# Kernel optimization log

Measured on AMD Instinct MI355X. Metric: run time of the kernel, lower is better.

Reference implementation:

```python
import jax, jax.numpy as jnp
import numpy as np

B = 128            # trees per batch
D = 6              # complete binary tree depth
NPT = 2 ** (D + 1) - 1   # 127 nodes per tree
H = 450            # JTNN hidden size
V = 780            # junction-tree vocab size


def _build_forest():
    # complete binary trees; node 0 of each tree is the root
    child = np.arange(1, NPT)
    parent = (child - 1) // 2
    offs = (np.arange(B) * NPT)[:, None]
    ch = (child[None, :] + offs).ravel()
    pa = (parent[None, :] + offs).ravel()
    Eup = B * (NPT - 1)
    E = 2 * Eup
    # up (child->parent) edges first, then down (parent->child); +1 dummy pad row
    src = np.concatenate([ch, pa, [0]]).astype(np.int32)
    dst = np.concatenate([pa, ch, [0]]).astype(np.int32)
    rev = np.concatenate([np.arange(Eup) + Eup, np.arange(Eup), [E]]).astype(np.int32)
    depth_child = np.floor(np.log2(child + 1)).astype(np.int64)  # 1..D
    toff = np.arange(B)[:, None] * (NPT - 1)
    rows = []
    for d in range(D, 0, -1):        # bottom-up: deepest child level first
        t = np.nonzero(depth_child == d)[0]
        rows.append((t[None, :] + toff).ravel())
    for d in range(1, D + 1):        # top-down
        t = np.nonzero(depth_child == d)[0]
        rows.append((t[None, :] + toff).ravel() + Eup)
    Lmax = max(len(r) for r in rows)
    sched = np.full((len(rows), Lmax), E, dtype=np.int32)   # pad with dummy id E
    for i, r in enumerate(rows):
        sched[i, :len(r)] = r
    return src, dst, rev, sched


def setup_inputs() -> dict:
    key = jax.random.key(0)
    ks = jax.random.split(key, 8)
    src, dst, rev, sched = _build_forest()
    n_nodes = B * NPT
    p = lambda k, shp: jax.random.normal(k, shp, jnp.float32) * 0.05
    return {
        'wid': jax.random.randint(ks[0], (n_nodes,), 0, V).astype(jnp.int32),
        'src': jnp.asarray(src), 'dst': jnp.asarray(dst), 'rev': jnp.asarray(rev),
        'sched': jnp.asarray(sched),
        'emb': p(ks[1], (V, H)),
        'Wz': p(ks[2], (2 * H, H)), 'bz': jnp.zeros((H,), jnp.float32),
        'Wr': p(ks[3], (H, H)),
        'Ur': p(ks[4], (H, H)), 'bur': jnp.zeros((H,), jnp.float32),
        'Wh': p(ks[5], (2 * H, H)), 'bh': jnp.zeros((H,), jnp.float32),
        'Wg': p(ks[6], (2 * H, H)), 'bg': jnp.zeros((H,), jnp.float32),
    }


def _forward(wid, src, dst, rev, sched, emb, Wz, bz, Wr, Ur, bur, Wh, bh, Wg, bg):
    n_nodes = wid.shape[0]
    E = src.shape[0] - 1              # last slot is a dummy pad row
    x = emb[wid]                      # [N, H] node embeddings
    m = jnp.zeros((E + 1, x.shape[1]), x.dtype)   # edge messages (line-graph node state)
    rm = jnp.zeros_like(m)
    dstE = dst[:E]
    for lvl in range(sched.shape[0]):             # static number of tree levels
        eid = sched[lvl]                          # [Lmax], padded with E
        # pull: s/accum_rm = sum over predecessor line-graph nodes, i.e.
        # sum of m over in-edges of src[e] minus the backtracking (reverse) edge
        node_m = jax.ops.segment_sum(m[:E], dstE, num_segments=n_nodes)
        node_rm = jax.ops.segment_sum(rm[:E], dstE, num_segments=n_nodes)
        se, de = src[eid], dst[eid]
        s = node_m[se] - m[rev[eid]]
        arm = node_rm[se] - rm[rev[eid]]
        sx, dx = x[se], x[de]
        # GRUUpdate (DGL JTNN)
        z = jax.nn.sigmoid(jnp.concatenate([sx, s], 1) @ Wz + bz)
        mt = jnp.tanh(jnp.concatenate([sx, arm], 1) @ Wh + bh)
        m_new = (1.0 - z) * s + z * mt
        r = jax.nn.sigmoid(dx @ Wr + m_new @ Ur + bur)   # W_r has no bias
        m = m.at[eid].set(m_new)
        rm = rm.at[eid].set(r * m_new)
    # update_all: gather messages into destination nodes, then EncoderGatherUpdate
    node_m = jax.ops.segment_sum(m[:E], dstE, num_segments=n_nodes)
    h = jax.nn.relu(jnp.concatenate([x, node_m], 1) @ Wg + bg)   # [N, H]
    return h


def reference(wid, src, dst, rev, sched, emb, Wz, bz, Wr, Ur, bur, Wh, bh, Wg, bg):
    # returns h for all nodes; root_vecs = h[node_offsets] (roots are every NPT-th node)
    return _forward(wid, src, dst, rev, sched, emb, Wz, bz, Wr, Ur, bur, Wh, bh, Wg, bg)
```

## Files before the change

kernel.cpp:

```cpp
#include <hip/hip_runtime.h>
#include <math.h>

#define NTREES 128
#define NPT 127
#define NNODES (NTREES*NPT)
#define EUP (NTREES*(NPT-1))
#define HDIM 450
#define HP 512
#define LMAX 8192
#define NLVL 12

typedef unsigned short u16;
typedef __attribute__((ext_vector_type(8))) short bf16x8;
typedef __attribute__((ext_vector_type(4))) float f32x4;

__device__ __forceinline__ float sigmoidf_(float x) { return 1.f / (1.f + expf(-x)); }
__device__ __forceinline__ u16 f2b(float x) {
  unsigned u = __float_as_uint(x);
  return (u16)((u + 0x7FFFu + ((u >> 16) & 1u)) >> 16);
}
__device__ __forceinline__ float b2f(u16 h) { return __uint_as_float(((unsigned)h) << 16); }
__device__ __forceinline__ bf16x8 sub8(bf16x8 a, bf16x8 b) {
  bf16x8 r;
#pragma unroll
  for (int i = 0; i < 8; ++i) r[i] = (short)f2b(b2f((u16)a[i]) - b2f((u16)b[i]));
  return r;
}

__device__ __forceinline__ u16* ldsp(u16* base, int row, int slot) {
  return base + row * 64 + ((slot ^ (row & 7)) << 3);
}
#define MFMA(a, b, c) __builtin_amdgcn_mfma_f32_16x16x32_bf16(a, b, c, 0, 0, 0)

__device__ __forceinline__ void swz_tiles(int bid, int Mt, int& nt, int& mt) {
  if (Mt & 7) { nt = bid & 7; mt = bid >> 3; }
  else { int xcd = bid & 7; int q = bid >> 3; nt = q & 7; mt = (q & ~7) | xcd; }
}

__global__ void zero_ws(float4* __restrict__ p, int n4) {
  int i = blockIdx.x * 256 + threadIdx.x;
  int stride = gridDim.x * 256;
  for (; i < n4; i += stride) p[i] = make_float4(0.f, 0.f, 0.f, 0.f);
}

__global__ void prep_pad(const float* __restrict__ Wz, const float* __restrict__ Wh,
                         const float* __restrict__ Wr, const float* __restrict__ Ur,
                         const float* __restrict__ Wg,
                         const float* __restrict__ bz, const float* __restrict__ bh,
                         const float* __restrict__ bur, const float* __restrict__ bg,
                         u16* __restrict__ WpreT, u16* __restrict__ WzbT,
                         u16* __restrict__ WhbT, u16* __restrict__ UrT,
                         u16* __restrict__ WgT, float* __restrict__ biasp) {
  int idx = blockIdx.x * 256 + threadIdx.x;
  if (idx < 1536 * 512) {
    int n = idx >> 9, k = idx & 511;
    int sel = n >> 9, j = n & 511;
    float v = 0.f;
    if (k < HDIM && j < HDIM) {
      const float* W = (sel == 0) ? Wz : (sel == 1) ? Wh : Wr;
      v = W[k * HDIM + j];
    }
    WpreT[idx] = f2b(v);
    return;
  }
  idx -= 1536 * 512;
  if (idx < 3 * 262144) {
    int which = idx >> 18; int r = idx & 262143;
    int n = r >> 9, k = r & 511;
    float v = 0.f;
    if (k < HDIM && n < HDIM)
      v = (which == 0) ? Wz[(HDIM + k) * HDIM + n]
        : (which == 1) ? Wh[(HDIM + k) * HDIM + n]
                       : Ur[k * HDIM + n];
    ((which == 0) ? WzbT : (which == 1) ? WhbT : UrT)[r] = f2b(v);
    return;
  }
  idx -= 3 * 262144;
  if (idx < 512 * 1024) {
    int n = idx >> 10, k = idx & 1023;
    float v = 0.f;
    if (n < HDIM) {
      if (k < HDIM) v = Wg[k * HDIM + n];
      else if (k >= HP && (k - HP) < HDIM) v = Wg[(HDIM + k - HP) * HDIM + n];
    }
    WgT[idx] = f2b(v);
    return;
  }
  idx -= 512 * 1024;
  if (idx < 4 * HP) {
    int which = idx >> 9, j = idx & 511;
    float v = 0.f;
    if (j < HDIM)
      v = ((which == 0) ? bz : (which == 1) ? bh : (which == 2) ? bur : bg)[j];
    biasp[idx] = v;
  }
}

__global__ void gather_embed(const int* __restrict__ wid, const float* __restrict__ emb,
                             u16* __restrict__ xp) {
  int gid = blockIdx.x * 256 + threadIdx.x;
  if (gid >= NNODES * 64) return;
  int row = gid >> 6, g = gid & 63;
  int j0 = g * 8;
  const float* er = emb + (size_t)wid[row] * HDIM;
  float f[8] = {0.f, 0.f, 0.f, 0.f, 0.f, 0.f, 0.f, 0.f};
  if (j0 <= 440) {
#pragma unroll
    for (int q = 0; q < 4; ++q) {
      float2 p = *(const float2*)(er + j0 + q * 2);
      f[q * 2] = p.x; f[q * 2 + 1] = p.y;
    }
  } else if (j0 == 448) {
    f[0] = er[448]; f[1] = er[449];
  }
  bf16x8 v;
#pragma unroll
  for (int q = 0; q < 8; ++q) v[q] = (short)f2b(f[q]);
  *(bf16x8*)(xp + (size_t)row * HP + j0) = v;
}

__global__ __launch_bounds__(256, 4) void mfma_pre(
    const u16* __restrict__ xp, const u16* __restrict__ WpreT,
    u16* __restrict__ Xzh, u16* __restrict__ Xr) {
  __shared__ u16 Al[64 * 64], Bl[64 * 64];
  int bid = blockIdx.x;
  int xcd = bid & 7, q0 = bid >> 3;
  int nt = q0 % 24;
  int mt = (q0 / 24) * 8 + xcd;
  if (mt >= NNODES / 64) return;
  int n0 = nt * 64, m0 = mt * 64;
  int tid = threadIdx.x;
  int l = tid & 63, w = tid >> 6, wr = w >> 1, wc = w & 1, lr = l & 15, lq = l >> 4;
  int sr = tid >> 2, skc = tid & 3;
  const u16* abase = xp + (size_t)(m0 + sr) * HP + skc * 16;
  const u16* bbase = WpreT + (size_t)(n0 + sr) * HP + skc * 16;
  f32x4 acc[2][2] = {};
  for (int kt = 0; kt < HP; kt += 64) {
    *(bf16x8*)ldsp(Al, sr, 2 * skc) = ((const bf16x8*)(abase + kt))[0];
    *(bf16x8*)ldsp(Al, sr, 2 * skc + 1) = ((const bf16x8*)(abase + kt))[1];
    *(bf16x8*)ldsp(Bl, sr, 2 * skc) = ((const bf16x8*)(bbase + kt))[0];
    *(bf16x8*)ldsp(Bl, sr, 2 * skc + 1) = ((const bf16x8*)(bbase + kt))[1];
    __syncthreads();
#pragma unroll
    for (int kk = 0; kk < 64; kk += 32) {
      int slot = (kk >> 3) + lq;
      bf16x8 fa0 = *(bf16x8*)ldsp(Al, wr * 32 + lr, slot);
      bf16x8 fa1 = *(bf16x8*)ldsp(Al, wr * 32 + 16 + lr, slot);
      bf16x8 fb0 = *(bf16x8*)ldsp(Bl, wc * 32 + lr, slot);
      bf16x8 fb1 = *(bf16x8*)ldsp(Bl, wc * 32 + 16 + lr, slot);
      acc[0][0] = MFMA(fa0, fb0, acc[0][0]); acc[0][1] = MFMA(fa0, fb1, acc[0][1]);
      acc[1][0] = MFMA(fa1, fb0, acc[1][0]); acc[1][1] = MFMA(fa1, fb1, acc[1][1]);
    }
    __syncthreads();
  }
#pragma unroll
  for (int fi = 0; fi < 2; ++fi)
#pragma unroll
    for (int fj = 0; fj < 2; ++fj) {
      int colg = n0 + wc * 32 + fj * 16 + lr;
#pragma unroll
      for (int reg = 0; reg < 4; ++reg) {
        int row = m0 + wr * 32 + fi * 16 + lq * 4 + reg;
        u16 o = f2b(acc[fi][fj][reg]);
        if (colg < 1024) Xzh[(size_t)row * 1024 + colg] = o;
        else Xr[(size_t)row * HP + (colg - 1024)] = o;
      }
    }
}

__global__ void leaf_lvl0(const int* __restrict__ sched0, const int* __restrict__ src,
                          const u16* __restrict__ Xzh, const float* __restrict__ biasp,
                          u16* __restrict__ mup) {
  int gid = blockIdx.x * 256 + threadIdx.x;
  int r = gid >> 7, g = gid & 127;
  int e = sched0[r];
  int se = src[e];
  int col = g * 4;
  ushort4 xz = *(const ushort4*)(Xzh + (size_t)se * 1024 + col);
  ushort4 xh = *(const ushort4*)(Xzh + (size_t)se * 1024 + 512 + col);
  float4 bz = *(const float4*)(biasp + col);
  float4 bh = *(const float4*)(biasp + 512 + col);
  ushort4 o;
  o.x = f2b(sigmoidf_(b2f(xz.x) + bz.x) * tanhf(b2f(xh.x) + bh.x));
  o.y = f2b(sigmoidf_(b2f(xz.y) + bz.y) * tanhf(b2f(xh.y) + bh.y));
  o.z = f2b(sigmoidf_(b2f(xz.z) + bz.z) * tanhf(b2f(xh.z) + bh.z));
  o.w = f2b(sigmoidf_(b2f(xz.w) + bz.w) * tanhf(b2f(xh.w) + bh.w));
  *(ushort4*)(mup + (size_t)e * HP + col) = o;
}

__global__ __launch_bounds__(256, 4) void mfma_lvl1_up(
    const int* __restrict__ schedrow, const int* __restrict__ src,
    const u16* __restrict__ node_m, const u16* __restrict__ node_rm,
    const u16* __restrict__ Xzh, const u16* __restrict__ WzbT,
    const u16* __restrict__ WhbT, const float* __restrict__ biasp,
    u16* __restrict__ mup) {
  __shared__ u16 Asl[64 * 64], Aal[64 * 64], Bzl[64 * 64], Btl[64 * 64];
  __shared__ int e_s[64], se_s[64];
  int nt, mt;
  swz_tiles(blockIdx.x, gridDim.x >> 3, nt, mt);
  int n0 = nt * 64, m0 = mt * 64;
  int tid = threadIdx.x;
  if (tid < 64) { int e = schedrow[m0 + tid]; e_s[tid] = e; se_s[tid] = src[e]; }
  __syncthreads();
  int l = tid & 63, w = tid >> 6, wr = w >> 1, wc = w & 1, lr = l & 15, lq = l >> 4;
  int sr = tid >> 2, skc = tid & 3;
  int se_st = se_s[sr];
  const u16* pmb = node_m + (size_t)se_st * HP + skc * 16;
  const u16* prb = node_rm + (size_t)se_st * HP + skc * 16;
  const u16* bzb = WzbT + (size_t)(n0 + sr) * HP + skc * 16;
  const u16* btb = WhbT + (size_t)(n0 + sr) * HP + skc * 16;
  f32x4 accZ[2][2] = {}, accT[2][2] = {};
  for (int kt = 0; kt < HP; kt += 64) {
    *(bf16x8*)ldsp(Asl, sr, 2 * skc) = ((const bf16x8*)(pmb + kt))[0];
    *(bf16x8*)ldsp(Asl, sr, 2 * skc + 1) = ((const bf16x8*)(pmb + kt))[1];
    *(bf16x8*)ldsp(Aal, sr, 2 * skc) = ((const bf16x8*)(prb + kt))[0];
    *(bf16x8*)ldsp(Aal, sr, 2 * skc + 1) = ((const bf16x8*)(prb + kt))[1];
    *(bf16x8*)ldsp(Bzl, sr, 2 * skc) = ((const bf16x8*)(bzb + kt))[0];
    *(bf16x8*)ldsp(Bzl, sr, 2 * skc + 1) = ((const bf16x8*)(bzb + kt))[1];
    *(bf16x8*)ldsp(Btl, sr, 2 * skc) = ((const bf16x8*)(btb + kt))[0];
    *(bf16x8*)ldsp(Btl, sr, 2 * skc + 1) = ((const bf16x8*)(btb + kt))[1];
    __syncthreads();
#pragma unroll
    for (int kk = 0; kk < 64; kk += 32) {
      int slot = (kk >> 3) + lq;
      bf16x8 a0 = *(bf16x8*)ldsp(Asl, wr * 32 + lr, slot);
      bf16x8 a1 = *(bf16x8*)ldsp(Asl, wr * 32 + 16 + lr, slot);
      bf16x8 c0 = *(bf16x8*)ldsp(Aal, wr * 32 + lr, slot);
      bf16x8 c1 = *(bf16x8*)ldsp(Aal, wr * 32 + 16 + lr, slot);
      bf16x8 z0 = *(bf16x8*)ldsp(Bzl, wc * 32 + lr, slot);
      bf16x8 z1 = *(bf16x8*)ldsp(Bzl, wc * 32 + 16 + lr, slot);
      bf16x8 t0 = *(bf16x8*)ldsp(Btl, wc * 32 + lr, slot);
      bf16x8 t1 = *(bf16x8*)ldsp(Btl, wc * 32 + 16 + lr, slot);
      accZ[0][0] = MFMA(a0, z0, accZ[0][0]); accZ[0][1] = MFMA(a0, z1, accZ[0][1]);
      accZ[1][0] = MFMA(a1, z0, accZ[1][0]); accZ[1][1] = MFMA(a1, z1, accZ[1][1]);
      accT[0][0] = MFMA(c0, t0, accT[0][0]); accT[0][1] = MFMA(c0, t1, accT[0][1]);
      accT[1][0] = MFMA(c1, t0, accT[1][0]); accT[1][1] = MFMA(c1, t1, accT[1][1]);
    }
    __syncthreads();
  }
#pragma unroll
  for (int fi = 0; fi < 2; ++fi)
#pragma unroll
    for (int fj = 0; fj < 2; ++fj) {
      int colg = n0 + wc * 32 + fj * 16 + lr;
#pragma unroll
      for (int reg = 0; reg < 4; ++reg) {
        int row = wr * 32 + fi * 16 + lq * 4 + reg;
        int e = e_s[row], se = se_s[row];
        float xz = b2f(Xzh[(size_t)se * 1024 + colg]);
        float xh = b2f(Xzh[(size_t)se * 1024 + 512 + colg]);
        float sv = b2f(node_m[(size_t)se * HP + colg]);
        float z = sigmoidf_(accZ[fi][fj][reg] + xz + biasp[colg]);
        float t = tanhf(accT[fi][fj][reg] + xh + biasp[512 + colg]);
        mup[(size_t)e * HP + colg] = f2b((1.f - z) * sv + z * t);
      }
    }
}

__global__ __launch_bounds__(256, 4) void mfma_lvl1_down(
    const int* __restrict__ schedrow, const int* __restrict__ src,
    const u16* __restrict__ node_m, const u16* __restrict__ node_rm,
    const u16* __restrict__ mup, const u16* __restrict__ rmup,
    const u16* __restrict__ Xzh, const u16* __restrict__ WzbT,
    const u16* __restrict__ WhbT, const float* __restrict__ biasp,
    u16* __restrict__ dtmp) {
  __shared__ u16 Asl[64 * 64], Aal[64 * 64], Bzl[64 * 64], Btl[64 * 64];
  __shared__ int se_s[64], eu_s[64];
  int nt, mt;
  swz_tiles(blockIdx.x, gridDim.x >> 3, nt, mt);
  int n0 = nt * 64, m0 = mt * 64;
  int tid = threadIdx.x;
  if (tid < 64) { int e = schedrow[m0 + tid]; eu_s[tid] = e - EUP; se_s[tid] = src[e]; }
  __syncthreads();
  int l = tid & 63, w = tid >> 6, wr = w >> 1, wc = w & 1, lr = l & 15, lq = l >> 4;
  int sr = tid >> 2, skc = tid & 3;
  int se_st = se_s[sr], eu_st = eu_s[sr];
  const u16* pmb = node_m + (size_t)se_st * HP + skc * 16;
  const u16* pub = mup + (size_t)eu_st * HP + skc * 16;
  const u16* prb = node_rm + (size_t)se_st * HP + skc * 16;
  const u16* pvb = rmup + (size_t)eu_st * HP + skc * 16;
  const u16* bzb = WzbT + (size_t)(n0 + sr) * HP + skc * 16;
  const u16* btb = WhbT + (size_t)(n0 + sr) * HP + skc * 16;
  f32x4 accZ[2][2] = {}, accT[2][2] = {};
  for (int kt = 0; kt < HP; kt += 64) {
    *(bf16x8*)ldsp(Asl, sr, 2 * skc) = sub8(((const bf16x8*)(pmb + kt))[0], ((const bf16x8*)(pub + kt))[0]);
    *(bf16x8*)ldsp(Asl, sr, 2 * skc + 1) = sub8(((const bf16x8*)(pmb + kt))[1], ((const bf16x8*)(pub + kt))[1]);
    *(bf16x8*)ldsp(Aal, sr, 2 * skc) = sub8(((const bf16x8*)(prb + kt))[0], ((const bf16x8*)(pvb + kt))[0]);
    *(bf16x8*)ldsp(Aal, sr, 2 * skc + 1) = sub8(((const bf16x8*)(prb + kt))[1], ((const bf16x8*)(pvb + kt))[1]);
    *(bf16x8*)ldsp(Bzl, sr, 2 * skc) = ((const bf16x8*)(bzb + kt))[0];
    *(bf16x8*)ldsp(Bzl, sr, 2 * skc + 1) = ((const bf16x8*)(bzb + kt))[1];
    *(bf16x8*)ldsp(Btl, sr, 2 * skc) = ((const bf16x8*)(btb + kt))[0];
    *(bf16x8*)ldsp(Btl, sr, 2 * skc + 1) = ((const bf16x8*)(btb + kt))[1];
    __syncthreads();
#pragma unroll
    for (int kk = 0; kk < 64; kk += 32) {
      int slot = (kk >> 3) + lq;
      bf16x8 a0 = *(bf16x8*)ldsp(Asl, wr * 32 + lr, slot);
      bf16x8 a1 = *(bf16x8*)ldsp(Asl, wr * 32 + 16 + lr, slot);
      bf16x8 c0 = *(bf16x8*)ldsp(Aal, wr * 32 + lr, slot);
      bf16x8 c1 = *(bf16x8*)ldsp(Aal, wr * 32 + 16 + lr, slot);
      bf16x8 z0 = *(bf16x8*)ldsp(Bzl, wc * 32 + lr, slot);
      bf16x8 z1 = *(bf16x8*)ldsp(Bzl, wc * 32 + 16 + lr, slot);
      bf16x8 t0 = *(bf16x8*)ldsp(Btl, wc * 32 + lr, slot);
      bf16x8 t1 = *(bf16x8*)ldsp(Btl, wc * 32 + 16 + lr, slot);
      accZ[0][0] = MFMA(a0, z0, accZ[0][0]); accZ[0][1] = MFMA(a0, z1, accZ[0][1]);
      accZ[1][0] = MFMA(a1, z0, accZ[1][0]); accZ[1][1] = MFMA(a1, z1, accZ[1][1]);
      accT[0][0] = MFMA(c0, t0, accT[0][0]); accT[0][1] = MFMA(c0, t1, accT[0][1]);
      accT[1][0] = MFMA(c1, t0, accT[1][0]); accT[1][1] = MFMA(c1, t1, accT[1][1]);
    }
    __syncthreads();
  }
#pragma unroll
  for (int fi = 0; fi < 2; ++fi)
#pragma unroll
    for (int fj = 0; fj < 2; ++fj) {
      int colg = n0 + wc * 32 + fj * 16 + lr;
#pragma unroll
      for (int reg = 0; reg < 4; ++reg) {
        int row = wr * 32 + fi * 16 + lq * 4 + reg;
        int se = se_s[row], eu = eu_s[row];
        float xz = b2f(Xzh[(size_t)se * 1024 + colg]);
        float xh = b2f(Xzh[(size_t)se * 1024 + 512 + colg]);
        float sv = b2f(node_m[(size_t)se * HP + colg]) - b2f(mup[(size_t)eu * HP + colg]);
        float z = sigmoidf_(accZ[fi][fj][reg] + xz + biasp[colg]);
        float t = tanhf(accT[fi][fj][reg] + xh + biasp[512 + colg]);
        dtmp[(size_t)(m0 + row) * HP + colg] = f2b((1.f - z) * sv + z * t);
      }
    }
}

__global__ __launch_bounds__(256, 4) void mfma_lvl2_up(
    const int* __restrict__ schedrow, const int* __restrict__ dst,
    const u16* __restrict__ mup, u16* __restrict__ rmup,
    u16* __restrict__ node_m, u16* __restrict__ node_rm,
    const u16* __restrict__ Xr, const u16* __restrict__ UrT,
    const float* __restrict__ biasp) {
  __shared__ u16 Al[64 * 64], Bl[64 * 64];
  __shared__ int e_s[64], de_s[64];
  int nt, mt;
  swz_tiles(blockIdx.x, gridDim.x >> 3, nt, mt);
  int n0 = nt * 64, m0 = mt * 64;
  int tid = threadIdx.x;
  if (tid < 64) { int e = schedrow[m0 + tid]; e_s[tid] = e; de_s[tid] = dst[e]; }
  __syncthreads();
  int l = tid & 63, w = tid >> 6, wr = w >> 1, wc = w & 1, lr = l & 15, lq = l >> 4;
  int sr = tid >> 2, skc = tid & 3;
  const u16* ab = mup + (size_t)e_s[sr] * HP + skc * 16;
  const u16* bb = UrT + (size_t)(n0 + sr) * HP + skc * 16;
  f32x4 acc[2][2] = {};
  for (int kt = 0; kt < HP; kt += 64) {
    *(bf16x8*)ldsp(Al, sr, 2 * skc) = ((const bf16x8*)(ab + kt))[0];
    *(bf16x8*)ldsp(Al, sr, 2 * skc + 1) = ((const bf16x8*)(ab + kt))[1];
    *(bf16x8*)ldsp(Bl, sr, 2 * skc) = ((const bf16x8*)(bb + kt))[0];
    *(bf16x8*)ldsp(Bl, sr, 2 * skc + 1) = ((const bf16x8*)(bb + kt))[1];
    __syncthreads();
#pragma unroll
    for (int kk = 0; kk < 64; kk += 32) {
      int slot = (kk >> 3) + lq;
      bf16x8 fa0 = *(bf16x8*)ldsp(Al, wr * 32 + lr, slot);
      bf16x8 fa1 = *(bf16x8*)ldsp(Al, wr * 32 + 16 + lr, slot);
      bf16x8 fb0 = *(bf16x8*)ldsp(Bl, wc * 32 + lr, slot);
      bf16x8 fb1 = *(bf16x8*)ldsp(Bl, wc * 32 + 16 + lr, slot);
      acc[0][0] = MFMA(fa0, fb0, acc[0][0]); acc[0][1] = MFMA(fa0, fb1, acc[0][1]);
      acc[1][0] = MFMA(fa1, fb0, acc[1][0]); acc[1][1] = MFMA(fa1, fb1, acc[1][1]);
    }
    __syncthreads();
  }
#pragma unroll
  for (int fi = 0; fi < 2; ++fi)
#pragma unroll
    for (int fj = 0; fj < 2; ++fj) {
      int colg = n0 + wc * 32 + fj * 16 + lr;
      int rowbase = wr * 32 + fi * 16 + lq * 4;
      float mv[4], rmv[4];
#pragma unroll
      for (int reg = 0; reg < 4; ++reg) {
        int row = rowbase + reg;
        int e = e_s[row], de = de_s[row];
        mv[reg] = b2f(mup[(size_t)e * HP + colg]);
        float r = sigmoidf_(acc[fi][fj][reg] + b2f(Xr[(size_t)de * HP + colg]) + biasp[1024 + colg]);
        rmv[reg] = r * mv[reg];
        rmup[(size_t)e * HP + colg] = f2b(rmv[reg]);
      }
      int de0 = de_s[rowbase], de2 = de_s[rowbase + 2];
      node_m[(size_t)de0 * HP + colg] = f2b(mv[0] + mv[1]);
      node_rm[(size_t)de0 * HP + colg] = f2b(rmv[0] + rmv[1]);
      node_m[(size_t)de2 * HP + colg] = f2b(mv[2] + mv[3]);
      node_rm[(size_t)de2 * HP + colg] = f2b(rmv[2] + rmv[3]);
    }
}

__global__ __launch_bounds__(256, 4) void mfma_lvl2_down(
    const int* __restrict__ schedrow, const int* __restrict__ dst,
    const u16* __restrict__ dtmp,
    u16* __restrict__ node_m, u16* __restrict__ node_rm,
    const u16* __restrict__ Xr, const u16* __restrict__ UrT,
    const float* __restrict__ biasp) {
  __shared__ u16 Al[64 * 64], Bl[64 * 64];
  __shared__ int de_s[64];
  int nt, mt;
  swz_tiles(blockIdx.x, gridDim.x >> 3, nt, mt);
  int n0 = nt * 64, m0 = mt * 64;
  int tid = threadIdx.x;
  if (tid < 64) de_s[tid] = dst[schedrow[m0 + tid]];
  __syncthreads();
  int l = tid & 63, w = tid >> 6, wr = w >> 1, wc = w & 1, lr = l & 15, lq = l >> 4;
  int sr = tid >> 2, skc = tid & 3;
  const u16* ab = dtmp + (size_t)(m0 + sr) * HP + skc * 16;
  const u16* bb = UrT + (size_t)(n0 + sr) * HP + skc * 16;
  f32x4 acc[2][2] = {};
  for (int kt = 0; kt < HP; kt += 64) {
    *(bf16x8*)ldsp(Al, sr, 2 * skc) = ((const bf16x8*)(ab + kt))[0];
    *(bf16x8*)ldsp(Al, sr, 2 * skc + 1) = ((const bf16x8*)(ab + kt))[1];
    *(bf16x8*)ldsp(Bl, sr, 2 * skc) = ((const bf16x8*)(bb + kt))[0];
    *(bf16x8*)ldsp(Bl, sr, 2 * skc + 1) = ((const bf16x8*)(bb + kt))[1];
    __syncthreads();
#pragma unroll
    for (int kk = 0; kk < 64; kk += 32) {
      int slot = (kk >> 3) + lq;
      bf16x8 fa0 = *(bf16x8*)ldsp(Al, wr * 32 + lr, slot);
      bf16x8 fa1 = *(bf16x8*)ldsp(Al, wr * 32 + 16 + lr, slot);
      bf16x8 fb0 = *(bf16x8*)ldsp(Bl, wc * 32 + lr, slot);
      bf16x8 fb1 = *(bf16x8*)ldsp(Bl, wc * 32 + 16 + lr, slot);
      acc[0][0] = MFMA(fa0, fb0, acc[0][0]); acc[0][1] = MFMA(fa0, fb1, acc[0][1]);
      acc[1][0] = MFMA(fa1, fb0, acc[1][0]); acc[1][1] = MFMA(fa1, fb1, acc[1][1]);
    }
    __syncthreads();
  }
#pragma unroll
  for (int fi = 0; fi < 2; ++fi)
#pragma unroll
    for (int fj = 0; fj < 2; ++fj) {
      int colg = n0 + wc * 32 + fj * 16 + lr;
#pragma unroll
      for (int reg = 0; reg < 4; ++reg) {
        int row = wr * 32 + fi * 16 + lq * 4 + reg;
        int de = de_s[row];
        size_t nidx = (size_t)de * HP + colg;
        float mv = b2f(dtmp[(size_t)(m0 + row) * HP + colg]);
        float r = sigmoidf_(acc[fi][fj][reg] + b2f(Xr[nidx]) + biasp[1024 + colg]);
        node_m[nidx] = f2b(b2f(node_m[nidx]) + mv);
        node_rm[nidx] = f2b(b2f(node_rm[nidx]) + r * mv);
      }
    }
}

__global__ __launch_bounds__(256, 4) void mfma_final(
    const u16* __restrict__ xp, const u16* __restrict__ node_m,
    const u16* __restrict__ WgT, const float* __restrict__ biasp,
    float* __restrict__ out) {
  __shared__ u16 Al[64 * 64], Bl[64 * 64];
  int bid = blockIdx.x;
  int xcd = bid & 7, q0 = bid >> 3;
  int nt = q0 % 8;
  int mt = (q0 / 8) * 8 + xcd;
  if (mt >= NNODES / 64) return;
  int n0 = nt * 64, m0 = mt * 64;
  int tid = threadIdx.x;
  int l = tid & 63, w = tid >> 6, wr = w >> 1, wc = w & 1, lr = l & 15, lq = l >> 4;
  int sr = tid >> 2, skc = tid & 3;
  const u16* axb = xp + (size_t)(m0 + sr) * HP + skc * 16;
  const u16* anb = node_m + (size_t)(m0 + sr) * HP + skc * 16;
  const u16* bb = WgT + (size_t)(n0 + sr) * 1024 + skc * 16;
  f32x4 acc[2][2] = {};
  for (int kt = 0; kt < 1024; kt += 64) {
    const u16* ap = (kt < HP) ? (axb + kt) : (anb + (kt - HP));
    *(bf16x8*)ldsp(Al, sr, 2 * skc) = ((const bf16x8*)ap)[0];
    *(bf16x8*)ldsp(Al, sr, 2 * skc + 1) = ((const bf16x8*)ap)[1];
    *(bf16x8*)ldsp(Bl, sr, 2 * skc) = ((const bf16x8*)(bb + kt))[0];
    *(bf16x8*)ldsp(Bl, sr, 2 * skc + 1) = ((const bf16x8*)(bb + kt))[1];
    __syncthreads();
#pragma unroll
    for (int kk = 0; kk < 64; kk += 32) {
      int slot = (kk >> 3) + lq;
      bf16x8 fa0 = *(bf16x8*)ldsp(Al, wr * 32 + lr, slot);
      bf16x8 fa1 = *(bf16x8*)ldsp(Al, wr * 32 + 16 + lr, slot);
      bf16x8 fb0 = *(bf16x8*)ldsp(Bl, wc * 32 + lr, slot);
      bf16x8 fb1 = *(bf16x8*)ldsp(Bl, wc * 32 + 16 + lr, slot);
      acc[0][0] = MFMA(fa0, fb0, acc[0][0]); acc[0][1] = MFMA(fa0, fb1, acc[0][1]);
      acc[1][0] = MFMA(fa1, fb0, acc[1][0]); acc[1][1] = MFMA(fa1, fb1, acc[1][1]);
    }
    __syncthreads();
  }
#pragma unroll
  for (int fi = 0; fi < 2; ++fi)
#pragma unroll
    for (int fj = 0; fj < 2; ++fj) {
      int colg = n0 + wc * 32 + fj * 16 + lr;
      if (colg >= HDIM) continue;
#pragma unroll
      for (int reg = 0; reg < 4; ++reg) {
        int row = m0 + wr * 32 + fi * 16 + lq * 4 + reg;
        float v = acc[fi][fj][reg] + biasp[1536 + colg];
        out[(size_t)row * HDIM + colg] = v > 0.f ? v : 0.f;
      }
    }
}

extern "C" void kernel_launch(void* const* d_in, const int* in_sizes, int n_in,
                              void* d_out, int out_size, void* d_ws, size_t ws_size,
                              hipStream_t stream) {
  const int* wid = (const int*)d_in[0];
  const int* src = (const int*)d_in[1];
  const int* dst = (const int*)d_in[2];
  const int* sched = (const int*)d_in[4];
  const float* emb = (const float*)d_in[5];
  const float* Wz = (const float*)d_in[6];
  const float* bz = (const float*)d_in[7];
  const float* Wr = (const float*)d_in[8];
  const float* Ur = (const float*)d_in[9];
  const float* bur = (const float*)d_in[10];
  const float* Wh = (const float*)d_in[11];
  const float* bh = (const float*)d_in[12];
  const float* Wg = (const float*)d_in[13];
  const float* bg = (const float*)d_in[14];
  float* out = (float*)d_out;
  float* ws = (float*)d_ws;

  size_t o = 0;
  u16* x_p = (u16*)(ws + o);     o += (size_t)NNODES * HP / 2;
  u16* Xzh = (u16*)(ws + o);     o += (size_t)NNODES * 1024 / 2;
  u16* Xr = (u16*)(ws + o);      o += (size_t)NNODES * HP / 2;
  u16* node_m = (u16*)(ws + o);  o += (size_t)NNODES * HP / 2;
  u16* node_rm = (u16*)(ws + o); o += (size_t)NNODES * HP / 2;
  u16* mup = (u16*)(ws + o);     o += (size_t)EUP * HP / 2;
  u16* rmup = (u16*)(ws + o);    o += (size_t)EUP * HP / 2;
  u16* dtmp = (u16*)(ws + o);    o += (size_t)LMAX * HP / 2;
  u16* WpreT = (u16*)(ws + o);   o += (size_t)1536 * HP / 2;
  u16* WzbT = (u16*)(ws + o);    o += (size_t)HP * HP / 2;
  u16* WhbT = (u16*)(ws + o);    o += (size_t)HP * HP / 2;
  u16* UrT = (u16*)(ws + o);     o += (size_t)HP * HP / 2;
  u16* WgT = (u16*)(ws + o);     o += (size_t)HP * 1024 / 2;
  float* biasp = ws + o;         o += (size_t)4 * HP;
  if (ws_size < o * sizeof(float)) return;

  size_t zbytes = (size_t)2 * NNODES * HP * 2;
  zero_ws<<<2048, 256, 0, stream>>>((float4*)node_m, (int)(zbytes / 16));

  int prep_elems = 1536 * 512 + 3 * 262144 + 512 * 1024 + 4 * HP;
  prep_pad<<<(prep_elems + 255) / 256, 256, 0, stream>>>(
      Wz, Wh, Wr, Ur, Wg, bz, bh, bur, bg, WpreT, WzbT, WhbT, UrT, WgT, biasp);

  gather_embed<<<(NNODES * 64 + 255) / 256, 256, 0, stream>>>(wid, emb, x_p);

  mfma_pre<<<256 * 24, 256, 0, stream>>>(x_p, WpreT, Xzh, Xr);

  for (int lvl = 0; lvl < NLVL; ++lvl) {
    int L = (lvl < 6) ? (LMAX >> lvl) : (256 << (lvl - 6));
    const int* schedrow = sched + (size_t)lvl * LMAX;
    if (lvl == 0) {
      leaf_lvl0<<<4096, 256, 0, stream>>>(schedrow, src, Xzh, biasp, mup);
    } else if (lvl < 6) {
      mfma_lvl1_up<<<8 * (L / 64), 256, 0, stream>>>(
          schedrow, src, node_m, node_rm, Xzh, WzbT, WhbT, biasp, mup);
    } else {
      mfma_lvl1_down<<<8 * (L / 64), 256, 0, stream>>>(
          schedrow, src, node_m, node_rm, mup, rmup, Xzh, WzbT, WhbT, biasp, dtmp);
    }
    if (lvl < 6) {
      mfma_lvl2_up<<<8 * (L / 64), 256, 0, stream>>>(
          schedrow, dst, mup, rmup, node_m, node_rm, Xr, UrT, biasp);
    } else {
      mfma_lvl2_down<<<8 * (L / 64), 256, 0, stream>>>(
          schedrow, dst, dtmp, node_m, node_rm, Xr, UrT, biasp);
    }
  }

  mfma_final<<<256 * 8, 256, 0, stream>>>(x_p, node_m, WgT, biasp, out);
}
```

Before: 557.8 us.

## Fuse per-level tree propagation kernels into one persistent cooperative kernel with grid barriers

Replaces the 24 per-level kernel launches for the bottom-up/top-down message passing with a single cooperative persistent kernel that loops over levels, distributes tile jobs across a capped grid and uses an atomic-counter grid barrier between phases. This is meant to remove launch overhead and tail gaps on the small late levels. In exchange each block must process several jobs serially at large levels, occupancy is lower (launch bounds 2), and spin barriers add latency. A fallback to the original multi-launch path remains if the cooperative launch fails.

```diff
diff --git a/kernel.cpp b/kernel.cpp
--- a/kernel.cpp
+++ b/kernel.cpp
@@ -9,6 +9,7 @@
 #define HP 512
 #define LMAX 8192
 #define NLVL 12
+#define CHAIN_BLOCKS 512
 
 typedef unsigned short u16;
 typedef __attribute__((ext_vector_type(8))) short bf16x8;
@@ -35,6 +36,20 @@
 __device__ __forceinline__ void swz_tiles(int bid, int Mt, int& nt, int& mt) {
   if (Mt & 7) { nt = bid & 7; mt = bid >> 3; }
   else { int xcd = bid & 7; int q = bid >> 3; nt = q & 7; mt = (q & ~7) | xcd; }
+}
+
+__device__ __forceinline__ void gbar(unsigned* cnt) {
+  __syncthreads();
+  if (threadIdx.x == 0) {
+    __threadfence();
+    unsigned old = __hip_atomic_fetch_add(cnt, 1u, __ATOMIC_ACQ_REL,
+                                          __HIP_MEMORY_SCOPE_AGENT);
+    unsigned target = (old / gridDim.x + 1u) * gridDim.x;
+    while (__hip_atomic_load(cnt, __ATOMIC_ACQUIRE, __HIP_MEMORY_SCOPE_AGENT) < target)
+      __builtin_amdgcn_s_sleep(8);
+    __threadfence();
+  }
+  __syncthreads();
 }
 
 __global__ void zero_ws(float4* __restrict__ p, int n4) {
@@ -168,38 +183,17 @@
     }
 }
 
-__global__ void leaf_lvl0(const int* __restrict__ sched0, const int* __restrict__ src,
-                          const u16* __restrict__ Xzh, const float* __restrict__ biasp,
-                          u16* __restrict__ mup) {
-  int gid = blockIdx.x * 256 + threadIdx.x;
-  int r = gid >> 7, g = gid & 127;
-  int e = sched0[r];
-  int se = src[e];
-  int col = g * 4;
-  ushort4 xz = *(const ushort4*)(Xzh + (size_t)se * 1024 + col);
-  ushort4 xh = *(const ushort4*)(Xzh + (size_t)se * 1024 + 512 + col);
-  float4 bz = *(const float4*)(biasp + col);
-  float4 bh = *(const float4*)(biasp + 512 + col);
-  ushort4 o;
-  o.x = f2b(sigmoidf_(b2f(xz.x) + bz.x) * tanhf(b2f(xh.x) + bh.x));
-  o.y = f2b(sigmoidf_(b2f(xz.y) + bz.y) * tanhf(b2f(xh.y) + bh.y));
-  o.z = f2b(sigmoidf_(b2f(xz.z) + bz.z) * tanhf(b2f(xh.z) + bh.z));
-  o.w = f2b(sigmoidf_(b2f(xz.w) + bz.w) * tanhf(b2f(xh.w) + bh.w));
-  *(ushort4*)(mup + (size_t)e * HP + col) = o;
-}
-
-__global__ __launch_bounds__(256, 4) void mfma_lvl1_up(
-    const int* __restrict__ schedrow, const int* __restrict__ src,
+__device__ __forceinline__ void job_lvl1_up(
+    int job, int Mt, const int* __restrict__ schedrow, const int* __restrict__ src,
     const u16* __restrict__ node_m, const u16* __restrict__ node_rm,
     const u16* __restrict__ Xzh, const u16* __restrict__ WzbT,
     const u16* __restrict__ WhbT, const float* __restrict__ biasp,
-    u16* __restrict__ mup) {
-  __shared__ u16 Asl[64 * 64], Aal[64 * 64], Bzl[64 * 64], Btl[64 * 64];
-  __shared__ int e_s[64], se_s[64];
-  int nt, mt;
-  swz_tiles(blockIdx.x, gridDim.x >> 3, nt, mt);
+    u16* __restrict__ mup,
+    u16* Asl, u16* Aal, u16* Bzl, u16* Btl, int* e_s, int* se_s) {
+  int tid = threadIdx.x;
+  int nt, mt; swz_tiles(job, Mt, nt, mt);
   int n0 = nt * 64, m0 = mt * 64;
-  int tid = threadIdx.x;
+  __syncthreads();
   if (tid < 64) { int e = schedrow[m0 + tid]; e_s[tid] = e; se_s[tid] = src[e]; }
   __syncthreads();
   int l = tid & 63, w = tid >> 6, wr = w >> 1, wc = w & 1, lr = l & 15, lq = l >> 4;
@@ -257,19 +251,18 @@
     }
 }
 
-__global__ __launch_bounds__(256, 4) void mfma_lvl1_down(
-    const int* __restrict__ schedrow, const int* __restrict__ src,
+__device__ __forceinline__ void job_lvl1_down(
+    int job, int Mt, const int* __restrict__ schedrow, const int* __restrict__ src,
     const u16* __restrict__ node_m, const u16* __restrict__ node_rm,
     const u16* __restrict__ mup, const u16* __restrict__ rmup,
     const u16* __restrict__ Xzh, const u16* __restrict__ WzbT,
     const u16* __restrict__ WhbT, const float* __restrict__ biasp,
-    u16* __restrict__ dtmp) {
-  __shared__ u16 Asl[64 * 64], Aal[64 * 64], Bzl[64 * 64], Btl[64 * 64];
-  __shared__ int se_s[64], eu_s[64];
-  int nt, mt;
-  swz_tiles(blockIdx.x, gridDim.x >> 3, nt, mt);
+    u16* __restrict__ dtmp,
+    u16* Asl, u16* Aal, u16* Bzl, u16* Btl, int* se_s, int* eu_s) {
+  int tid = threadIdx.x;
+  int nt, mt; swz_tiles(job, Mt, nt, mt);
   int n0 = nt * 64, m0 = mt * 64;
-  int tid = threadIdx.x;
+  __syncthreads();
   if (tid < 64) { int e = schedrow[m0 + tid]; eu_s[tid] = e - EUP; se_s[tid] = src[e]; }
   __syncthreads();
   int l = tid & 63, w = tid >> 6, wr = w >> 1, wc = w & 1, lr = l & 15, lq = l >> 4;
@@ -329,18 +322,17 @@
     }
 }
 
-__global__ __launch_bounds__(256, 4) void mfma_lvl2_up(
-    const int* __restrict__ schedrow, const int* __restrict__ dst,
+__device__ __forceinline__ void job_lvl2_up(
+    int job, int Mt, const int* __restrict__ schedrow, const int* __restrict__ dst,
     const u16* __restrict__ mup, u16* __restrict__ rmup,
     u16* __restrict__ node_m, u16* __restrict__ node_rm,
     const u16* __restrict__ Xr, const u16* __restrict__ UrT,
-    const float* __restrict__ biasp) {
-  __shared__ u16 Al[64 * 64], Bl[64 * 64];
-  __shared__ int e_s[64], de_s[64];
-  int nt, mt;
-  swz_tiles(blockIdx.x, gridDim.x >> 3, nt, mt);
+    const float* __restrict__ biasp,
+    u16* Al, u16* Bl, int* e_s, int* de_s) {
+  int tid = threadIdx.x;
+  int nt, mt; swz_tiles(job, Mt, nt, mt);
   int n0 = nt * 64, m0 = mt * 64;
-  int tid = threadIdx.x;
+  __syncthreads();
   if (tid < 64) { int e = schedrow[m0 + tid]; e_s[tid] = e; de_s[tid] = dst[e]; }
   __syncthreads();
   int l = tid & 63, w = tid >> 6, wr = w >> 1, wc = w & 1, lr = l & 15, lq = l >> 4;
@@ -390,18 +382,16 @@
     }
 }
 
-__global__ __launch_bounds__(256, 4) void mfma_lvl2_down(
-    const int* __restrict__ schedrow, const int* __restrict__ dst,
-    const u16* __restrict__ dtmp,
-    u16* __restrict__ node_m, u16* __restrict__ node_rm,
+__device__ __forceinline__ void job_lvl2_down(
+    int job, int Mt, const int* __restrict__ schedrow, const int* __restrict__ dst,
+    const u16* __restrict__ dtmp, u16* __restrict__ node_m, u16* __restrict__ node_rm,
     const u16* __restrict__ Xr, const u16* __restrict__ UrT,
-    const float* __restrict__ biasp) {
-  __shared__ u16 Al[64 * 64], Bl[64 * 64];
-  __shared__ int de_s[64];
-  int nt, mt;
-  swz_tiles(blockIdx.x, gridDim.x >> 3, nt, mt);
+    const float* __restrict__ biasp,
+    u16* Al, u16* Bl, int* de_s) {
+  int tid = threadIdx.x;
+  int nt, mt; swz_tiles(job, Mt, nt, mt);
   int n0 = nt * 64, m0 = mt * 64;
-  int tid = threadIdx.x;
+  __syncthreads();
   if (tid < 64) de_s[tid] = dst[schedrow[m0 + tid]];
   __syncthreads();
   int l = tid & 63, w = tid >> 6, wr = w >> 1, wc = w & 1, lr = l & 15, lq = l >> 4;
@@ -443,6 +433,131 @@
         node_rm[nidx] = f2b(b2f(node_rm[nidx]) + r * mv);
       }
     }
+}
+
+__global__ __launch_bounds__(256, 2) void level_chain(
+    const int* __restrict__ sched, const int* __restrict__ src,
+    const int* __restrict__ dst,
+    u16* __restrict__ node_m, u16* __restrict__ node_rm,
+    u16* __restrict__ mup, u16* __restrict__ rmup, u16* __restrict__ dtmp,
+    const u16* __restrict__ Xzh, const u16* __restrict__ Xr,
+    const u16* __restrict__ WzbT, const u16* __restrict__ WhbT,
+    const u16* __restrict__ UrT, const float* __restrict__ biasp,
+    unsigned* gcnt) {
+  __shared__ u16 T0[64 * 64], T1[64 * 64], T2[64 * 64], T3[64 * 64];
+  __shared__ int i0[64], i1[64];
+  int tid = threadIdx.x;
+  for (int lvl = 0; lvl < NLVL; ++lvl) {
+    int L = (lvl < 6) ? (LMAX >> lvl) : (256 << (lvl - 6));
+    const int* schedrow = sched + (size_t)lvl * LMAX;
+    int Mt = L / 64, jobs = 8 * Mt;
+    if (lvl == 0) {
+      for (int gid = blockIdx.x * 256 + tid; gid < LMAX * 64; gid += gridDim.x * 256) {
+        int r = gid >> 6, q = gid & 63;
+        int e = schedrow[r];
+        int se = src[e];
+        int col = q * 8;
+        bf16x8 vz = *(const bf16x8*)(Xzh + (size_t)se * 1024 + col);
+        bf16x8 vh = *(const bf16x8*)(Xzh + (size_t)se * 1024 + 512 + col);
+        bf16x8 o;
+#pragma unroll
+        for (int k = 0; k < 8; ++k) {
+          float z = sigmoidf_(b2f((u16)vz[k]) + biasp[col + k]);
+          float t = tanhf(b2f((u16)vh[k]) + biasp[512 + col + k]);
+          o[k] = (short)f2b(z * t);
+        }
+        *(bf16x8*)(mup + (size_t)e * HP + col) = o;
+      }
+    } else if (lvl < 6) {
+      for (int job = blockIdx.x; job < jobs; job += gridDim.x)
+        job_lvl1_up(job, Mt, schedrow, src, node_m, node_rm, Xzh, WzbT, WhbT,
+                    biasp, mup, T0, T1, T2, T3, i0, i1);
+    } else {
+      for (int job = blockIdx.x; job < jobs; job += gridDim.x)
+        job_lvl1_down(job, Mt, schedrow, src, node_m, node_rm, mup, rmup, Xzh,
+                      WzbT, WhbT, biasp, dtmp, T0, T1, T2, T3, i0, i1);
+    }
+    gbar(gcnt);
+    if (lvl < 6) {
+      for (int job = blockIdx.x; job < jobs; job += gridDim.x)
+        job_lvl2_up(job, Mt, schedrow, dst, mup, rmup, node_m, node_rm, Xr, UrT,
+                    biasp, T0, T1, i0, i1);
+    } else {
+      for (int job = blockIdx.x; job < jobs; job += gridDim.x)
+        job_lvl2_down(job, Mt, schedrow, dst, dtmp, node_m, node_rm, Xr, UrT,
+                      biasp, T0, T1, i0);
+    }
+    gbar(gcnt);
+  }
+}
+
+__global__ void leaf_lvl0(const int* __restrict__ sched0, const int* __restrict__ src,
+                          const u16* __restrict__ Xzh, const float* __restrict__ biasp,
+                          u16* __restrict__ mup) {
+  int gid = blockIdx.x * 256 + threadIdx.x;
+  int r = gid >> 7, g = gid & 127;
+  int e = sched0[r];
+  int se = src[e];
+  int col = g * 4;
+  ushort4 xz = *(const ushort4*)(Xzh + (size_t)se * 1024 + col);
+  ushort4 xh = *(const ushort4*)(Xzh + (size_t)se * 1024 + 512 + col);
+  float4 bz = *(const float4*)(biasp + col);
+  float4 bh = *(const float4*)(biasp + 512 + col);
+  ushort4 o;
+  o.x = f2b(sigmoidf_(b2f(xz.x) + bz.x) * tanhf(b2f(xh.x) + bh.x));
+  o.y = f2b(sigmoidf_(b2f(xz.y) + bz.y) * tanhf(b2f(xh.y) + bh.y));
+  o.z = f2b(sigmoidf_(b2f(xz.z) + bz.z) * tanhf(b2f(xh.z) + bh.z));
+  o.w = f2b(sigmoidf_(b2f(xz.w) + bz.w) * tanhf(b2f(xh.w) + bh.w));
+  *(ushort4*)(mup + (size_t)e * HP + col) = o;
+}
+
+__global__ __launch_bounds__(256, 4) void mfma_lvl1_up(
+    const int* __restrict__ schedrow, const int* __restrict__ src,
+    const u16* __restrict__ node_m, const u16* __restrict__ node_rm,
+    const u16* __restrict__ Xzh, const u16* __restrict__ WzbT,
+    const u16* __restrict__ WhbT, const float* __restrict__ biasp,
+    u16* __restrict__ mup) {
+  __shared__ u16 T0[64 * 64], T1[64 * 64], T2[64 * 64], T3[64 * 64];
+  __shared__ int i0[64], i1[64];
+  job_lvl1_up(blockIdx.x, gridDim.x >> 3, schedrow, src, node_m, node_rm, Xzh,
+              WzbT, WhbT, biasp, mup, T0, T1, T2, T3, i0, i1);
+}
+
+__global__ __launch_bounds__(256, 4) void mfma_lvl1_down(
+    const int* __restrict__ schedrow, const int* __restrict__ src,
+    const u16* __restrict__ node_m, const u16* __restrict__ node_rm,
+    const u16* __restrict__ mup, const u16* __restrict__ rmup,
+    const u16* __restrict__ Xzh, const u16* __restrict__ WzbT,
+    const u16* __restrict__ WhbT, const float* __restrict__ biasp,
+    u16* __restrict__ dtmp) {
+  __shared__ u16 T0[64 * 64], T1[64 * 64], T2[64 * 64], T3[64 * 64];
+  __shared__ int i0[64], i1[64];
+  job_lvl1_down(blockIdx.x, gridDim.x >> 3, schedrow, src, node_m, node_rm, mup,
+                rmup, Xzh, WzbT, WhbT, biasp, dtmp, T0, T1, T2, T3, i0, i1);
+}
+
+__global__ __launch_bounds__(256, 4) void mfma_lvl2_up(
+    const int* __restrict__ schedrow, const int* __restrict__ dst,
+    const u16* __restrict__ mup, u16* __restrict__ rmup,
+    u16* __restrict__ node_m, u16* __restrict__ node_rm,
+    const u16* __restrict__ Xr, const u16* __restrict__ UrT,
+    const float* __restrict__ biasp) {
+  __shared__ u16 T0[64 * 64], T1[64 * 64];
+  __shared__ int i0[64], i1[64];
+  job_lvl2_up(blockIdx.x, gridDim.x >> 3, schedrow, dst, mup, rmup, node_m,
+              node_rm, Xr, UrT, biasp, T0, T1, i0, i1);
+}
+
+__global__ __launch_bounds__(256, 4) void mfma_lvl2_down(
+    const int* __restrict__ schedrow, const int* __restrict__ dst,
+    const u16* __restrict__ dtmp,
+    u16* __restrict__ node_m, u16* __restrict__ node_rm,
+    const u16* __restrict__ Xr, const u16* __restrict__ UrT,
+    const float* __restrict__ biasp) {
+  __shared__ u16 T0[64 * 64], T1[64 * 64];
+  __shared__ int i0[64];
+  job_lvl2_down(blockIdx.x, gridDim.x >> 3, schedrow, dst, dtmp, node_m,
+                node_rm, Xr, UrT, biasp, T0, T1, i0);
 }
 
 __global__ __launch_bounds__(256, 4) void mfma_final(
@@ -523,6 +638,7 @@
   u16* Xr = (u16*)(ws + o);      o += (size_t)NNODES * HP / 2;
   u16* node_m = (u16*)(ws + o);  o += (size_t)NNODES * HP / 2;
   u16* node_rm = (u16*)(ws + o); o += (size_t)NNODES * HP / 2;
+  unsigned* gcnt = (unsigned*)(ws + o); o += 16;
   u16* mup = (u16*)(ws + o);     o += (size_t)EUP * HP / 2;
   u16* rmup = (u16*)(ws + o);    o += (size_t)EUP * HP / 2;
   u16* dtmp = (u16*)(ws + o);    o += (size_t)LMAX * HP / 2;
@@ -534,7 +650,7 @@
   float* biasp = ws + o;         o += (size_t)4 * HP;
   if (ws_size < o * sizeof(float)) return;
 
-  size_t zbytes = (size_t)2 * NNODES * HP * 2;
+  size_t zbytes = (size_t)2 * NNODES * HP * 2 + 64;
   zero_ws<<<2048, 256, 0, stream>>>((float4*)node_m, (int)(zbytes / 16));
 
   int prep_elems = 1536 * 512 + 3 * 262144 + 512 * 1024 + 4 * HP;
@@ -545,24 +661,55 @@
 
   mfma_pre<<<256 * 24, 256, 0, stream>>>(x_p, WpreT, Xzh, Xr);
 
-  for (int lvl = 0; lvl < NLVL; ++lvl) {
-    int L = (lvl < 6) ? (LMAX >> lvl) : (256 << (lvl - 6));
-    const int* schedrow = sched + (size_t)lvl * LMAX;
-    if (lvl == 0) {
-      leaf_lvl0<<<4096, 256, 0, stream>>>(schedrow, src, Xzh, biasp, mup);
-    } else if (lvl < 6) {
-      mfma_lvl1_up<<<8 * (L / 64), 256, 0, stream>>>(
-          schedrow, src, node_m, node_rm, Xzh, WzbT, WhbT, biasp, mup);
-    } else {
-      mfma_lvl1_down<<<8 * (L / 64), 256, 0, stream>>>(
-          schedrow, src, node_m, node_rm, mup, rmup, Xzh, WzbT, WhbT, biasp, dtmp);
-    }
-    if (lvl < 6) {
-      mfma_lvl2_up<<<8 * (L / 64), 256, 0, stream>>>(
-          schedrow, dst, mup, rmup, node_m, node_rm, Xr, UrT, biasp);
-    } else {
-      mfma_lvl2_down<<<8 * (L / 64), 256, 0, stream>>>(
-          schedrow, dst, dtmp, node_m, node_rm, Xr, UrT, biasp);
+  hipError_t ce = hipErrorUnknown;
+  {
+    int dev = 0; hipGetDevice(&dev);
+    int coop = 0;
+    hipDeviceGetAttribute(&coop, hipDeviceAttributeCooperativeLaunch, dev);
+    int numCU = 0;
+    hipDeviceGetAttribute(&numCU, hipDeviceAttributeMultiprocessorCount, dev);
+    int perCU = 0;
+    hipOccupancyMaxActiveBlocksPerMultiprocessor(&perCU, (const void*)level_chain,
+                                                 256, 0);
+    int grid_n = perCU * numCU;
+    if (grid_n > CHAIN_BLOCKS) grid_n = CHAIN_BLOCKS;
+    if (coop && grid_n >= 8) {
+      const int* sched_a = sched; const int* src_a = src; const int* dst_a = dst;
+      u16* node_m_a = node_m; u16* node_rm_a = node_rm;
+      u16* mup_a = mup; u16* rmup_a = rmup; u16* dtmp_a = dtmp;
+      const u16* Xzh_a = Xzh; const u16* Xr_a = Xr;
+      const u16* WzbT_a = WzbT; const u16* WhbT_a = WhbT; const u16* UrT_a = UrT;
+      const float* biasp_a = biasp; unsigned* gcnt_a = gcnt;
+      void* args[] = {(void*)&sched_a, (void*)&src_a, (void*)&dst_a,
+                      (void*)&node_m_a, (void*)&node_rm_a,
+                      (void*)&mup_a, (void*)&rmup_a, (void*)&dtmp_a,
+                      (void*)&Xzh_a, (void*)&Xr_a,
+                      (void*)&WzbT_a, (void*)&WhbT_a, (void*)&UrT_a,
+                      (void*)&biasp_a, (void*)&gcnt_a};
+      ce = hipLaunchCooperativeKernel((const void*)level_chain, dim3(grid_n),
+                                      dim3(256), args, 0, stream);
+    }
+  }
+  if (ce != hipSuccess) {
+    for (int lvl = 0; lvl < NLVL; ++lvl) {
+      int L = (lvl < 6) ? (LMAX >> lvl) : (256 << (lvl - 6));
+      const int* schedrow = sched + (size_t)lvl * LMAX;
+      if (lvl == 0) {
+        leaf_lvl0<<<4096, 256, 0, stream>>>(schedrow, src, Xzh, biasp, mup);
+      } else if (lvl < 6) {
+        mfma_lvl1_up<<<8 * (L / 64), 256, 0, stream>>>(
+            schedrow, src, node_m, node_rm, Xzh, WzbT, WhbT, biasp, mup);
+      } else {
+        mfma_lvl1_down<<<8 * (L / 64), 256, 0, stream>>>(
+            schedrow, src, node_m, node_rm, mup, rmup, Xzh, WzbT, WhbT, biasp, dtmp);
+      }
+      if (lvl < 6) {
+        mfma_lvl2_up<<<8 * (L / 64), 256, 0, stream>>>(
+            schedrow, dst, mup, rmup, node_m, node_rm, Xr, UrT, biasp);
+      } else {
+        mfma_lvl2_down<<<8 * (L / 64), 256, 0, stream>>>(
+            schedrow, dst, dtmp, node_m, node_rm, Xr, UrT, biasp);
+      }
     }
   }
 
```

Result: slower. 1.818 ms (+226.0%).
